# Optimization experiments

Measured on AMD Instinct MI355X. Metric: run time of the kernel, lower is better.

Reference implementation:

```python
import jax, jax.numpy as jnp
import numpy as np

NUM_GROUPS = 32
EPS = 1e-5


def _conv(x, w, b, pad):
    # x: [B,C,H,W], w: [O,I,kh,kw]
    y = jax.lax.conv_general_dilated(
        x, w, window_strides=(1, 1), padding=[(pad, pad), (pad, pad)],
        dimension_numbers=('NCHW', 'OIHW', 'NCHW'))
    return y + b[None, :, None, None]


def _group_norm(x, gamma, beta):
    B, C, H, W = x.shape
    g = x.reshape(B, NUM_GROUPS, C // NUM_GROUPS, H, W)
    mu = g.mean(axis=(2, 3, 4), keepdims=True)
    var = g.var(axis=(2, 3, 4), keepdims=True)
    g = (g - mu) * jax.lax.rsqrt(var + EPS)
    x = g.reshape(B, C, H, W)
    return x * gamma[None, :, None, None] + beta[None, :, None, None]


def setup_inputs() -> dict:
    key = jax.random.key(0)
    ks = jax.random.split(key, 8)
    B, C, H, W = 8, 384, 64, 64
    s1 = 1.0 / np.sqrt(C)          # 1x1 conv fan-in
    s3 = 1.0 / np.sqrt(C * 9)      # 3x3 conv fan-in
    return {
        'x': jax.random.normal(ks[0], (B, C, H, W), dtype=jnp.float32),
        'gamma': jnp.ones((C,), dtype=jnp.float32),
        'beta': jnp.zeros((C,), dtype=jnp.float32),
        'wq': jax.random.normal(ks[1], (C, C, 1, 1), dtype=jnp.float32) * s1,
        'bq': jnp.zeros((C,), dtype=jnp.float32),
        'wk': jax.random.normal(ks[2], (C, C, 3, 3), dtype=jnp.float32) * s3,
        'bk': jnp.zeros((C,), dtype=jnp.float32),
        'wv': jax.random.normal(ks[3], (C, C, 1, 1), dtype=jnp.float32) * s1,
        'bv': jnp.zeros((C,), dtype=jnp.float32),
        'wf': jax.random.normal(ks[4], (C, C, 1, 1), dtype=jnp.float32) * s1,
        'bf': jnp.zeros((C,), dtype=jnp.float32),
        'k': 512,
    }


def reference(x, gamma, beta, wq, bq, wk, bk, wv, bv, wf, bf, k):
    B, C, H, W = x.shape
    xn = _group_norm(x, gamma, beta)
    q = _conv(xn, wq, bq, 0)
    kk = _conv(xn, wk, bk, 1)
    v = _conv(xn, wv, bv, 0)
    # frequency-domain correlation: elementwise product of 2D spectra
    Fq = jnp.fft.fft2(q)
    Fk = jnp.fft.fft2(kk)
    A = jnp.fft.ifft2(Fq * Fk).real          # [B,C,H,W]
    # per-(batch,channel) spatial top-k sparsification
    A_flat = A.reshape(B, C, H * W)
    topv, _ = jax.lax.top_k(A_flat, k)
    thresh = topv[..., -1:]                   # k-th largest value
    masked = jnp.where(A_flat >= thresh, A_flat, -jnp.inf)
    Fw = jax.nn.softmax(masked, axis=-1).reshape(B, C, H, W)
    F4 = v * Fw                               # weighted values
    res = _conv(F4, wf, bf, 0)
    return xn * res
```

## Files before the change

### kernel.cpp

```cpp
#include <hip/hip_runtime.h>
#include <hip/hip_fp16.h>
#include <math.h>

#define CCH  384
#define BATCH 8
#define HWN  4096
#define NG   32
#define CPG  12
#define KSEL 512
#define FFTP 65
#define LP   40

typedef short v8s  __attribute__((ext_vector_type(8)));
typedef float v16f __attribute__((ext_vector_type(16)));

#define MFMA_B16(A_,B_,C_) __builtin_amdgcn_mfma_f32_32x32x16_bf16((A_),(B_),(C_),0,0,0)

__device__ __forceinline__ unsigned br6(unsigned i) {
  return ((i&1u)<<5)|((i&2u)<<3)|((i&4u)<<1)|((i&8u)>>1)|((i&16u)>>3)|((i&32u)>>5);
}
__device__ __forceinline__ unsigned f2key(float f) {
  unsigned u = __float_as_uint(f);
  return (u & 0x80000000u) ? ~u : (u | 0x80000000u);
}
__device__ __forceinline__ float wave_max(float v) {
#pragma unroll
  for (int o = 32; o > 0; o >>= 1) v = fmaxf(v, __shfl_down(v, o, 64));
  return v;
}
__device__ __forceinline__ float wave_sum(float v) {
#pragma unroll
  for (int o = 32; o > 0; o >>= 1) v += __shfl_down(v, o, 64);
  return v;
}
__device__ __forceinline__ unsigned short bf16_rne(float f) {
  unsigned u = __float_as_uint(f);
  return (unsigned short)((u + 0x7fffu + ((u >> 16) & 1u)) >> 16);
}
__device__ __forceinline__ float bf2f(unsigned short h) {
  return __uint_as_float(((unsigned)h) << 16);
}

__global__ __launch_bounds__(256) void stats_kernel(const float* __restrict__ x,
                                                    float2* __restrict__ gs) {
  int b = blockIdx.x >> 5, g = blockIdx.x & 31;
  size_t base = ((size_t)b * CCH + (size_t)g * CPG) * HWN;
  const float4* xp = (const float4*)(x + base);
  int tid = threadIdx.x;
  const int N4 = CPG * HWN / 4;
  float s = 0.f, ss = 0.f;
  for (int i = tid; i < N4; i += 256) {
    float4 v = xp[i];
    s  += (v.x + v.y) + (v.z + v.w);
    ss += (v.x*v.x + v.y*v.y) + (v.z*v.z + v.w*v.w);
  }
  s = wave_sum(s); ss = wave_sum(ss);
  __shared__ float sb[4], qb[4];
  if ((tid & 63) == 0) { sb[tid >> 6] = s; qb[tid >> 6] = ss; }
  __syncthreads();
  if (tid == 0) {
    float S = sb[0]+sb[1]+sb[2]+sb[3], Q = qb[0]+qb[1]+qb[2]+qb[3];
    float inv = 1.0f / (float)(CPG * HWN);
    float mu = S * inv;
    float var = Q * inv - mu * mu;
    gs[blockIdx.x] = make_float2(mu, rsqrtf(var + 1e-5f));
  }
}

__global__ __launch_bounds__(256) void pack_split_k(const float* __restrict__ w,
    unsigned short* __restrict__ hi, unsigned short* __restrict__ lo, int n) {
  int i = blockIdx.x * 256 + threadIdx.x;
  if (i >= n) return;
  float f = w[i];
  unsigned short h = bf16_rne(f);
  hi[i] = h;
  lo[i] = bf16_rne(f - bf2f(h));
}
__global__ __launch_bounds__(256) void pack9_k(const float* __restrict__ w,
    unsigned short* __restrict__ hi, unsigned short* __restrict__ lo) {
  int i = blockIdx.x * 256 + threadIdx.x;
  int r = blockIdx.y;
  float f = w[(size_t)i * 9 + r];
  unsigned short h = bf16_rne(f);
  size_t o = (size_t)r * 147456 + i;
  hi[o] = h;
  lo[o] = bf16_rne(f - bf2f(h));
}

template<int FUSE, int SPLIT>
__global__ __launch_bounds__(256) void trans_kernel(const float* __restrict__ in,
    const float2* __restrict__ gs, const float* __restrict__ gamma,
    const float* __restrict__ beta,
    unsigned short* __restrict__ oh, unsigned short* __restrict__ ol) {
  __shared__ float ts[64][65];
  int tid = threadIdx.x;
  int b = blockIdx.z, c0 = blockIdx.y * 64, p0 = blockIdx.x * 64;
#pragma unroll
  for (int i = 0; i < 4; ++i) {
    int idx = tid + (i << 8);
    int row = idx >> 4, col = (idx & 15) << 2;
    float4 v = *(const float4*)&in[((size_t)b*CCH + c0 + row)*HWN + p0 + col];
    if (FUSE) {
      int c = c0 + row;
      float2 st = gs[(b << 5) + c / CPG];
      float a = gamma[c] * st.y, bb = beta[c] - st.x * a;
      v.x = v.x*a+bb; v.y = v.y*a+bb; v.z = v.z*a+bb; v.w = v.w*a+bb;
    }
    ts[row][col] = v.x; ts[row][col+1] = v.y; ts[row][col+2] = v.z; ts[row][col+3] = v.w;
  }
  __syncthreads();
#pragma unroll
  for (int i = 0; i < 2; ++i) {
    int idx = tid + (i << 8);
    int p = idx >> 3, cgp = (idx & 7) << 3;
    unsigned short h8[8] __attribute__((aligned(16)));
    unsigned short l8[8] __attribute__((aligned(16)));
#pragma unroll
    for (int j = 0; j < 8; ++j) {
      float f = ts[cgp + j][p];
      unsigned short hb = bf16_rne(f);
      h8[j] = hb;
      if (SPLIT) l8[j] = bf16_rne(f - bf2f(hb));
    }
    size_t o = ((size_t)b*HWN + p0 + p)*CCH + c0 + cgp;
    *(uint4*)&oh[o] = *(const uint4*)h8;
    if (SPLIT) *(uint4*)&ol[o] = *(const uint4*)l8;
  }
}

template<int TAPS, int OUT>
__global__ __launch_bounds__(256, 3) void mm_kernel(
    const unsigned short* __restrict__ Ahg, const unsigned short* __restrict__ Alg,
    const float* __restrict__ bias,
    const unsigned short* __restrict__ Bhg, const unsigned short* __restrict__ Blg,
    const unsigned short* __restrict__ xnTh, const unsigned short* __restrict__ xnTl,
    void* __restrict__ Yv) {
  __shared__ unsigned short Ah_s[128*LP], Al_s[128*LP], Bh_s[128*LP], Bl_s[128*LP];
  int tid = threadIdx.x;
  int b = blockIdx.z, m0 = blockIdx.y * 128, n0 = blockIdx.x * 128;
  int y0 = blockIdx.x * 2;
  int u0row = tid >> 2, cg = tid & 3;
  int lds0 = u0row * LP + cg * 8, lds1 = lds0 + 64 * LP;
  size_t aoff0 = (size_t)(m0 + u0row) * CCH + cg * 8;
  int lane = tid & 63, wm = tid >> 7, wn = (tid >> 6) & 1;
  int lm = lane & 31, lh = lane >> 5;
  int arow = (wm * 64 + lm) * LP, brow = (wn * 64 + lm) * LP;

  v16f acc[2][2];
#pragma unroll
  for (int t = 0; t < 2; ++t)
#pragma unroll
    for (int s = 0; s < 2; ++s)
#pragma unroll
      for (int g = 0; g < 16; ++g) acc[t][s][g] = 0.f;

  const int NS = TAPS * 12;
  uint4 ra0h, ra0l, ra1h, ra1l, rb0h, rb0l, rb1h, rb1l;

  auto issue = [&](int s) {
    int r  = (TAPS == 9) ? (s / 12) : 0;
    int c0 = (s - r * 12) * 32;
    const unsigned short* Arh = Ahg + (size_t)r * CCH * CCH + aoff0 + c0;
    const unsigned short* Arl = Alg + (size_t)r * CCH * CCH + aoff0 + c0;
    ra0h = *(const uint4*)Arh;
    ra0l = *(const uint4*)Arl;
    ra1h = *(const uint4*)(Arh + 64 * CCH);
    ra1l = *(const uint4*)(Arl + 64 * CCH);
    int dy = (TAPS == 9) ? r / 3 - 1 : 0;
    int dx = (TAPS == 9) ? r % 3 - 1 : 0;
    int px = u0row + dx;
    int py0 = y0 + dy, py1 = py0 + 1;
    bool okx = (unsigned)px < 64u;
    bool ok0 = okx && ((unsigned)py0 < 64u);
    bool ok1 = okx && ((unsigned)py1 < 64u);
    size_t boff0 = ((size_t)b * HWN + py0 * 64 + px) * CCH + cg * 8 + c0;
    size_t boff1 = ((size_t)b * HWN + py1 * 64 + px) * CCH + cg * 8 + c0;
    uint4 zf; zf.x = zf.y = zf.z = zf.w = 0u;
    rb0h = ok0 ? *(const uint4*)(Bhg + boff0) : zf;
    rb0l = ok0 ? *(const uint4*)(Blg + boff0) : zf;
    rb1h = ok1 ? *(const uint4*)(Bhg + boff1) : zf;
    rb1l = ok1 ? *(const uint4*)(Blg + boff1) : zf;
  };

  issue(0);
  for (int s = 0; s < NS; ++s) {
    __syncthreads();
    *(uint4*)&Ah_s[lds0] = ra0h; *(uint4*)&Al_s[lds0] = ra0l;
    *(uint4*)&Ah_s[lds1] = ra1h; *(uint4*)&Al_s[lds1] = ra1l;
    *(uint4*)&Bh_s[lds0] = rb0h; *(uint4*)&Bl_s[lds0] = rb0l;
    *(uint4*)&Bh_s[lds1] = rb1h; *(uint4*)&Bl_s[lds1] = rb1l;
    __syncthreads();
    if (s + 1 < NS) issue(s + 1);
#pragma unroll
    for (int h = 0; h < 2; ++h) {
      int co = h * 16 + lh * 8;
      v8s a0h = *(const v8s*)&Ah_s[arow + co];
      v8s a1h = *(const v8s*)&Ah_s[arow + 32*LP + co];
      v8s a0l = *(const v8s*)&Al_s[arow + co];
      v8s a1l = *(const v8s*)&Al_s[arow + 32*LP + co];
      v8s b0h = *(const v8s*)&Bh_s[brow + co];
      v8s b1h = *(const v8s*)&Bh_s[brow + 32*LP + co];
      v8s b0l = *(const v8s*)&Bl_s[brow + co];
      v8s b1l = *(const v8s*)&Bl_s[brow + 32*LP + co];
      acc[0][0] = MFMA_B16(a0h, b0h, acc[0][0]);
      acc[0][0] = MFMA_B16(a0h, b0l, acc[0][0]);
      acc[0][0] = MFMA_B16(a0l, b0h, acc[0][0]);
      acc[0][1] = MFMA_B16(a0h, b1h, acc[0][1]);
      acc[0][1] = MFMA_B16(a0h, b1l, acc[0][1]);
      acc[0][1] = MFMA_B16(a0l, b1h, acc[0][1]);
      acc[1][0] = MFMA_B16(a1h, b0h, acc[1][0]);
      acc[1][0] = MFMA_B16(a1h, b0l, acc[1][0]);
      acc[1][0] = MFMA_B16(a1l, b0h, acc[1][0]);
      acc[1][1] = MFMA_B16(a1h, b1h, acc[1][1]);
      acc[1][1] = MFMA_B16(a1h, b1l, acc[1][1]);
      acc[1][1] = MFMA_B16(a1l, b1h, acc[1][1]);
    }
  }
#pragma unroll
  for (int t = 0; t < 2; ++t) {
    int mb = m0 + wm * 64 + t * 32;
#pragma unroll
    for (int s = 0; s < 2; ++s) {
      int n = n0 + wn * 64 + s * 32 + lm;
#pragma unroll
      for (int g = 0; g < 16; ++g) {
        int m = mb + (g & 3) + ((g >> 2) << 3) + (lh << 2);
        float val = acc[t][s][g] + bias[m];
        size_t oidx = ((size_t)b * CCH + m) * HWN + n;
        if (OUT == 0) {
          ((float*)Yv)[oidx] = val;
        } else if (OUT == 1) {
          ((__half*)Yv)[oidx] = __float2half(val);
        } else {
          size_t tix = ((size_t)b * HWN + n) * CCH + m;
          float xnv = bf2f(xnTh[tix]) + bf2f(xnTl[tix]);
          ((float*)Yv)[oidx] = val * xnv;
        }
      }
    }
  }
}

__device__ __forceinline__ void fft4_pass(float* zr, float* zi,
    const float* twr, const float* twi, int tid, int axis, float ds) {
#pragma unroll
  for (int s = 0; s < 3; ++s) {
    const int h = 1 << (2 * s);
#pragma unroll
    for (int tt = 0; tt < 4; ++tt) {
      int t = tid + (tt << 8);
      int line = t >> 4, bf = t & 15;
      int j  = bf & (h - 1);
      int i0 = ((bf >> (2 * s)) << (2 * s + 2)) + j;
      int e1 = j << (5 - 2 * s);
      int e2 = j << (4 - 2 * s);
      float w1r = twr[e1], w1i = ds * twi[e1];
      float w2r = twr[e2], w2i = ds * twi[e2];
      int A0, st;
      if (axis == 0) { A0 = line * FFTP + i0; st = h; }
      else           { A0 = i0 * FFTP + line; st = h * FFTP; }
      int A1 = A0 + st, A2 = A1 + st, A3 = A2 + st;
      float x0r = zr[A0], x0i = zi[A0];
      float x1r = zr[A1], x1i = zi[A1];
      float x2r = zr[A2], x2i = zi[A2];
      float x3r = zr[A3], x3i = zi[A3];
      float t1r = x1r*w1r - x1i*w1i, t1i = x1r*w1i + x1i*w1r;
      float t3r = x3r*w1r - x3i*w1i, t3i = x3r*w1i + x3i*w1r;
      float u0r = x0r + t1r, u0i = x0i + t1i;
      float u1r = x0r - t1r, u1i = x0i - t1i;
      float u2r = x2r + t3r, u2i = x2i + t3i;
      float u3r = x2r - t3r, u3i = x2i - t3i;
      float c2r = u2r*w2r - u2i*w2i, c2i = u2r*w2i + u2i*w2r;
      float c3r = u3r*w2r - u3i*w2i, c3i = u3r*w2i + u3i*w2r;
      zr[A0] = u0r + c2r;      zi[A0] = u0i + c2i;
      zr[A2] = u0r - c2r;      zi[A2] = u0i - c2i;
      zr[A1] = u1r + ds*c3i;   zi[A1] = u1i - ds*c3r;
      zr[A3] = u1r - ds*c3i;   zi[A3] = u1i + ds*c3r;
    }
    __syncthreads();
  }
}

__global__ __launch_bounds__(256) void fft_topk_kernel(
    const float* q, const float* __restrict__ kkb,
    const __half* __restrict__ v, float* F4) {
  __shared__ float zr[64 * FFTP], zi[64 * FFTP];
  __shared__ float twr[32], twi[32];
  __shared__ unsigned hist[256];
  __shared__ unsigned su2[2];
  __shared__ unsigned wtot[4];
  __shared__ float sred[5];
  int tid = threadIdx.x;
  int lane = tid & 63, w = tid >> 6;
  size_t base = (size_t)blockIdx.x * HWN;
  for (int i = tid; i < HWN; i += 256) {
    int y = i >> 6, x = i & 63;
    int slot = br6(y) * FFTP + br6(x);
    zr[slot] = q[base + i];
    zi[slot] = kkb[base + i];
  }
  if (tid < 32) {
    float ang = (float)tid * 0.0981747704246810387f;
    twr[tid] = cosf(ang);
    twi[tid] = -sinf(ang);
  }
  __syncthreads();
  fft4_pass(zr, zi, twr, twi, tid, 0, 1.f);
  fft4_pass(zr, zi, twr, twi, tid, 1, 1.f);
  float prr[16], pir[16];
#pragma unroll
  for (int c = 0; c < 16; c++) {
    int i = tid + (c << 8);
    int ky = i >> 6, kx = i & 63;
    float sr = zr[ky * FFTP + kx], si = zi[ky * FFTP + kx];
    int kyn = (64 - ky) & 63, kxn = (64 - kx) & 63;
    float nr = zr[kyn * FFTP + kxn], ni = zi[kyn * FFTP + kxn];
    float fqr = 0.5f * (sr + nr), fqi = 0.5f * (si - ni);
    float fkr = 0.5f * (si + ni), fki = 0.5f * (nr - sr);
    prr[c] = fqr * fkr - fqi * fki;
    pir[c] = fqr * fki + fqi * fkr;
  }
  __syncthreads();
#pragma unroll
  for (int c = 0; c < 16; c++) {
    int i = tid + (c << 8);
    int ky = i >> 6, kx = i & 63;
    int slot = br6(ky) * FFTP + br6(kx);
    zr[slot] = prr[c];
    zi[slot] = pir[c];
  }
  __syncthreads();
  fft4_pass(zr, zi, twr, twi, tid, 0, -1.f);
  fft4_pass(zr, zi, twr, twi, tid, 1, -1.f);
  const float scale = 1.0f / 4096.0f;
  float a[16];
  unsigned key[16];
  float mx = -3.0e38f;
#pragma unroll
  for (int c = 0; c < 16; c++) {
    int i = tid + (c << 8);
    a[c] = zr[(i >> 6) * FFTP + (i & 63)] * scale;
    key[c] = f2key(a[c]);
    mx = fmaxf(mx, a[c]);
  }
  mx = wave_max(mx);
  if (lane == 0) sred[w] = mx;
  __syncthreads();
  if (tid == 0) sred[4] = fmaxf(fmaxf(sred[0], sred[1]), fmaxf(sred[2], sred[3]));
  __syncthreads();
  float am = sred[4];
  unsigned prefix = 0; int kr = KSEL;
  for (int pass = 0; pass < 4; pass++) {
    int shift = 24 - (pass << 3);
    hist[tid] = 0;
    __syncthreads();
#pragma unroll
    for (int c = 0; c < 16; c++) {
      unsigned u = key[c];
      if (((u ^ prefix) >> shift) <= 0xFFu)
        atomicAdd(&hist[(u >> shift) & 255u], 1u);
    }
    __syncthreads();
    unsigned xv = hist[tid];
#pragma unroll
    for (int o = 1; o < 64; o <<= 1) {
      unsigned t2 = __shfl_down(xv, o, 64);
      if (lane + o < 64) xv += t2;
    }
    if (lane == 0) wtot[w] = xv;
    __syncthreads();
    for (int ww = w + 1; ww < 4; ++ww) xv += wtot[ww];
    hist[tid] = xv;
    __syncthreads();
    unsigned sv = xv;
    unsigned svn = (tid < 255) ? hist[tid + 1] : 0u;
    if (sv >= (unsigned)kr && svn < (unsigned)kr) { su2[0] = (unsigned)tid; su2[1] = svn; }
    __syncthreads();
    prefix |= su2[0] << shift;
    kr -= (int)su2[1];
  }
  unsigned thr = prefix;
  float lsum = 0.f;
#pragma unroll
  for (int c = 0; c < 16; c++)
    if (key[c] >= thr) lsum += expf(a[c] - am);
  lsum = wave_sum(lsum);
  if (lane == 0) sred[w] = lsum;
  __syncthreads();
  if (tid == 0) sred[4] = 1.0f / (sred[0] + sred[1] + sred[2] + sred[3]);
  __syncthreads();
  float inv = sred[4];
#pragma unroll
  for (int c = 0; c < 16; c++) {
    int i = tid + (c << 8);
    float wgt = (key[c] >= thr) ? expf(a[c] - am) * inv : 0.f;
    F4[base + i] = __half2float(v[base + i]) * wgt;
  }
}

extern "C" void kernel_launch(void* const* d_in, const int* in_sizes, int n_in,
                              void* d_out, int out_size, void* d_ws, size_t ws_size,
                              hipStream_t stream) {
  const float* x     = (const float*)d_in[0];
  const float* gamma = (const float*)d_in[1];
  const float* beta  = (const float*)d_in[2];
  const float* wq    = (const float*)d_in[3];
  const float* bq    = (const float*)d_in[4];
  const float* wk    = (const float*)d_in[5];
  const float* bk    = (const float*)d_in[6];
  const float* wv    = (const float*)d_in[7];
  const float* bv    = (const float*)d_in[8];
  const float* wf    = (const float*)d_in[9];
  const float* bf    = (const float*)d_in[10];

  const size_t NEL = (size_t)BATCH * CCH * HWN;
  const size_t WSZ = (size_t)CCH * CCH;

  unsigned short* xnTh = (unsigned short*)d_ws;
  unsigned short* xnTl = xnTh + NEL;
  float*  qC  = (float*)(xnTl + NEL);
  float*  kD  = qC + NEL;
  __half* vE  = (__half*)(kD + NEL);
  unsigned short* W = (unsigned short*)(vE + NEL);
  unsigned short* Wqh = W;
  unsigned short* Wql = Wqh + WSZ;
  unsigned short* Wvh = Wql + WSZ;
  unsigned short* Wvl = Wvh + WSZ;
  unsigned short* Wfh = Wvl + WSZ;
  unsigned short* Wfl = Wfh + WSZ;
  unsigned short* Wkh = Wfl + WSZ;
  unsigned short* Wkl = Wkh + 9 * WSZ;
  float2* gs = (float2*)(Wkl + 9 * WSZ);
  unsigned short* F4Th = (unsigned short*)kD;
  unsigned short* F4Tl = F4Th + NEL;

  pack_split_k<<<dim3(576), dim3(256), 0, stream>>>(wq, Wqh, Wql, (int)WSZ);
  pack_split_k<<<dim3(576), dim3(256), 0, stream>>>(wv, Wvh, Wvl, (int)WSZ);
  pack_split_k<<<dim3(576), dim3(256), 0, stream>>>(wf, Wfh, Wfl, (int)WSZ);
  pack9_k<<<dim3(576, 9), dim3(256), 0, stream>>>(wk, Wkh, Wkl);
  stats_kernel<<<dim3(BATCH * NG), dim3(256), 0, stream>>>(x, gs);
  trans_kernel<1, 1><<<dim3(64, 6, BATCH), dim3(256), 0, stream>>>(
      x, gs, gamma, beta, xnTh, xnTl);

  dim3 gm(32, 3, BATCH);
  mm_kernel<1, 0><<<gm, dim3(256), 0, stream>>>(Wqh, Wql, bq, xnTh, xnTl,
                                                nullptr, nullptr, qC);
  mm_kernel<9, 0><<<gm, dim3(256), 0, stream>>>(Wkh, Wkl, bk, xnTh, xnTl,
                                                nullptr, nullptr, kD);
  mm_kernel<1, 1><<<gm, dim3(256), 0, stream>>>(Wvh, Wvl, bv, xnTh, xnTl,
                                                nullptr, nullptr, vE);

  fft_topk_kernel<<<dim3(BATCH * CCH), dim3(256), 0, stream>>>(qC, kD, vE, qC);

  trans_kernel<0, 1><<<dim3(64, 6, BATCH), dim3(256), 0, stream>>>(
      qC, nullptr, nullptr, nullptr, F4Th, F4Tl);

  mm_kernel<1, 2><<<gm, dim3(256), 0, stream>>>(Wfh, Wfl, bf, F4Th, F4Tl,
                                                xnTh, xnTl, d_out);
}
```

Measured before the change: 694.3 us.

## Pre-pack weights in MFMA fragment order and load A operands straight to registers

Weights are now packed into per-lane MFMA fragment order, so each wave loads its A operands directly from global memory into registers. This removes the A tiles from shared memory and from the per-step LDS store and read traffic. The next step's A fragments are double-buffered in registers through a two-step unrolled loop. This raises register pressure, so the occupancy hint drops from 3 to 2 blocks. A fragments are also loaded separately by each wave rather than shared across waves through LDS.

```diff
diff --git a/kernel.cpp b/kernel.cpp
--- a/kernel.cpp
+++ b/kernel.cpp
@@ -67,24 +67,20 @@
   }
 }
 
-__global__ __launch_bounds__(256) void pack_split_k(const float* __restrict__ w,
-    unsigned short* __restrict__ hi, unsigned short* __restrict__ lo, int n) {
-  int i = blockIdx.x * 256 + threadIdx.x;
-  if (i >= n) return;
-  float f = w[i];
-  unsigned short h = bf16_rne(f);
-  hi[i] = h;
-  lo[i] = bf16_rne(f - bf2f(h));
-}
-__global__ __launch_bounds__(256) void pack9_k(const float* __restrict__ w,
-    unsigned short* __restrict__ hi, unsigned short* __restrict__ lo) {
-  int i = blockIdx.x * 256 + threadIdx.x;
+__global__ __launch_bounds__(256) void pack_frag_k(const float* __restrict__ w,
+    unsigned short* __restrict__ hi, unsigned short* __restrict__ lo, int taps) {
+  int idx = blockIdx.x * 256 + threadIdx.x;
   int r = blockIdx.y;
-  float f = w[(size_t)i * 9 + r];
-  unsigned short h = bf16_rne(f);
-  size_t o = (size_t)r * 147456 + i;
+  int f = idx >> 9;
+  int l = (idx >> 3) & 63, j = idx & 7;
+  int mb = f / 24, kc = f - mb * 24;
+  int m = mb * 32 + (l & 31);
+  int k = kc * 16 + ((l >> 5) << 3) + j;
+  float fv = (taps == 9) ? w[(size_t)(m * CCH + k) * 9 + r] : w[m * CCH + k];
+  unsigned short h = bf16_rne(fv);
+  size_t o = (size_t)r * 147456 + idx;
   hi[o] = h;
-  lo[o] = bf16_rne(f - bf2f(h));
+  lo[o] = bf16_rne(fv - bf2f(h));
 }
 
 template<int FUSE, int SPLIT>
@@ -129,22 +125,22 @@
 }
 
 template<int TAPS, int OUT>
-__global__ __launch_bounds__(256, 3) void mm_kernel(
+__global__ __launch_bounds__(256, 2) void mm_kernel(
     const unsigned short* __restrict__ Ahg, const unsigned short* __restrict__ Alg,
     const float* __restrict__ bias,
     const unsigned short* __restrict__ Bhg, const unsigned short* __restrict__ Blg,
     const unsigned short* __restrict__ xnTh, const unsigned short* __restrict__ xnTl,
     void* __restrict__ Yv) {
-  __shared__ unsigned short Ah_s[128*LP], Al_s[128*LP], Bh_s[128*LP], Bl_s[128*LP];
+  __shared__ unsigned short Bh_s[128*LP], Bl_s[128*LP];
   int tid = threadIdx.x;
   int b = blockIdx.z, m0 = blockIdx.y * 128, n0 = blockIdx.x * 128;
+  int mb0 = blockIdx.y * 4;
   int y0 = blockIdx.x * 2;
   int u0row = tid >> 2, cg = tid & 3;
   int lds0 = u0row * LP + cg * 8, lds1 = lds0 + 64 * LP;
-  size_t aoff0 = (size_t)(m0 + u0row) * CCH + cg * 8;
   int lane = tid & 63, wm = tid >> 7, wn = (tid >> 6) & 1;
   int lm = lane & 31, lh = lane >> 5;
-  int arow = (wm * 64 + lm) * LP, brow = (wn * 64 + lm) * LP;
+  int brow = (wn * 64 + lm) * LP;
 
   v16f acc[2][2];
 #pragma unroll
@@ -155,17 +151,12 @@
       for (int g = 0; g < 16; ++g) acc[t][s][g] = 0.f;
 
   const int NS = TAPS * 12;
-  uint4 ra0h, ra0l, ra1h, ra1l, rb0h, rb0l, rb1h, rb1l;
-
-  auto issue = [&](int s) {
+  uint4 rb0h, rb0l, rb1h, rb1l;
+  v8s A0[8], A1[8];
+
+  auto issueB = [&](int s) {
     int r  = (TAPS == 9) ? (s / 12) : 0;
     int c0 = (s - r * 12) * 32;
-    const unsigned short* Arh = Ahg + (size_t)r * CCH * CCH + aoff0 + c0;
-    const unsigned short* Arl = Alg + (size_t)r * CCH * CCH + aoff0 + c0;
-    ra0h = *(const uint4*)Arh;
-    ra0l = *(const uint4*)Arl;
-    ra1h = *(const uint4*)(Arh + 64 * CCH);
-    ra1l = *(const uint4*)(Arl + 64 * CCH);
     int dy = (TAPS == 9) ? r / 3 - 1 : 0;
     int dx = (TAPS == 9) ? r % 3 - 1 : 0;
     int px = u0row + dx;
@@ -181,41 +172,57 @@
     rb1h = ok1 ? *(const uint4*)(Bhg + boff1) : zf;
     rb1l = ok1 ? *(const uint4*)(Blg + boff1) : zf;
   };
-
-  issue(0);
-  for (int s = 0; s < NS; ++s) {
-    __syncthreads();
-    *(uint4*)&Ah_s[lds0] = ra0h; *(uint4*)&Al_s[lds0] = ra0l;
-    *(uint4*)&Ah_s[lds1] = ra1h; *(uint4*)&Al_s[lds1] = ra1l;
-    *(uint4*)&Bh_s[lds0] = rb0h; *(uint4*)&Bl_s[lds0] = rb0l;
-    *(uint4*)&Bh_s[lds1] = rb1h; *(uint4*)&Bl_s[lds1] = rb1l;
-    __syncthreads();
-    if (s + 1 < NS) issue(s + 1);
-#pragma unroll
-    for (int h = 0; h < 2; ++h) {
-      int co = h * 16 + lh * 8;
-      v8s a0h = *(const v8s*)&Ah_s[arow + co];
-      v8s a1h = *(const v8s*)&Ah_s[arow + 32*LP + co];
-      v8s a0l = *(const v8s*)&Al_s[arow + co];
-      v8s a1l = *(const v8s*)&Al_s[arow + 32*LP + co];
-      v8s b0h = *(const v8s*)&Bh_s[brow + co];
-      v8s b1h = *(const v8s*)&Bh_s[brow + 32*LP + co];
-      v8s b0l = *(const v8s*)&Bl_s[brow + co];
-      v8s b1l = *(const v8s*)&Bl_s[brow + 32*LP + co];
-      acc[0][0] = MFMA_B16(a0h, b0h, acc[0][0]);
-      acc[0][0] = MFMA_B16(a0h, b0l, acc[0][0]);
-      acc[0][0] = MFMA_B16(a0l, b0h, acc[0][0]);
-      acc[0][1] = MFMA_B16(a0h, b1h, acc[0][1]);
-      acc[0][1] = MFMA_B16(a0h, b1l, acc[0][1]);
-      acc[0][1] = MFMA_B16(a0l, b1h, acc[0][1]);
-      acc[1][0] = MFMA_B16(a1h, b0h, acc[1][0]);
-      acc[1][0] = MFMA_B16(a1h, b0l, acc[1][0]);
-      acc[1][0] = MFMA_B16(a1l, b0h, acc[1][0]);
-      acc[1][1] = MFMA_B16(a1h, b1h, acc[1][1]);
-      acc[1][1] = MFMA_B16(a1h, b1l, acc[1][1]);
-      acc[1][1] = MFMA_B16(a1l, b1h, acc[1][1]);
-    }
-  }
+  auto issueA = [&](int s, v8s* An) {
+    int r   = (TAPS == 9) ? (s / 12) : 0;
+    int kc0 = (s - r * 12) * 2;
+#pragma unroll
+    for (int t = 0; t < 2; ++t)
+#pragma unroll
+      for (int h = 0; h < 2; ++h) {
+        size_t f = (size_t)((r * 12 + mb0 + wm * 2 + t) * 24 + kc0 + h);
+        An[(t*2+h)*2+0] = *(const v8s*)(Ahg + (f << 9) + (lane << 3));
+        An[(t*2+h)*2+1] = *(const v8s*)(Alg + (f << 9) + (lane << 3));
+      }
+  };
+
+#define MMSTEP(SS, Acur, Anext)                                              \
+  {                                                                          \
+    __syncthreads();                                                         \
+    *(uint4*)&Bh_s[lds0] = rb0h; *(uint4*)&Bl_s[lds0] = rb0l;                \
+    *(uint4*)&Bh_s[lds1] = rb1h; *(uint4*)&Bl_s[lds1] = rb1l;                \
+    __syncthreads();                                                         \
+    if ((SS) + 1 < NS) { issueB((SS) + 1); issueA((SS) + 1, Anext); }        \
+    _Pragma("unroll")                                                        \
+    for (int h = 0; h < 2; ++h) {                                            \
+      int co = h * 16 + lh * 8;                                              \
+      v8s a0h = Acur[(0*2+h)*2+0], a0l = Acur[(0*2+h)*2+1];                  \
+      v8s a1h = Acur[(1*2+h)*2+0], a1l = Acur[(1*2+h)*2+1];                  \
+      v8s b0h = *(const v8s*)&Bh_s[brow + co];                               \
+      v8s b1h = *(const v8s*)&Bh_s[brow + 32*LP + co];                       \
+      v8s b0l = *(const v8s*)&Bl_s[brow + co];                               \
+      v8s b1l = *(const v8s*)&Bl_s[brow + 32*LP + co];                       \
+      acc[0][0] = MFMA_B16(a0h, b0h, acc[0][0]);                             \
+      acc[0][0] = MFMA_B16(a0h, b0l, acc[0][0]);                             \
+      acc[0][0] = MFMA_B16(a0l, b0h, acc[0][0]);                             \
+      acc[0][1] = MFMA_B16(a0h, b1h, acc[0][1]);                             \
+      acc[0][1] = MFMA_B16(a0h, b1l, acc[0][1]);                             \
+      acc[0][1] = MFMA_B16(a0l, b1h, acc[0][1]);                             \
+      acc[1][0] = MFMA_B16(a1h, b0h, acc[1][0]);                             \
+      acc[1][0] = MFMA_B16(a1h, b0l, acc[1][0]);                             \
+      acc[1][0] = MFMA_B16(a1l, b0h, acc[1][0]);                             \
+      acc[1][1] = MFMA_B16(a1h, b1h, acc[1][1]);                             \
+      acc[1][1] = MFMA_B16(a1h, b1l, acc[1][1]);                             \
+      acc[1][1] = MFMA_B16(a1l, b1h, acc[1][1]);                             \
+    }                                                                        \
+  }
+
+  issueB(0); issueA(0, A0);
+  for (int s = 0; s < NS; s += 2) {
+    MMSTEP(s, A0, A1);
+    MMSTEP(s + 1, A1, A0);
+  }
+#undef MMSTEP
+
 #pragma unroll
   for (int t = 0; t < 2; ++t) {
     int mb = m0 + wm * 64 + t * 32;
@@ -256,14 +263,14 @@
       int e2 = j << (4 - 2 * s);
       float w1r = twr[e1], w1i = ds * twi[e1];
       float w2r = twr[e2], w2i = ds * twi[e2];
-      int A0, st;
-      if (axis == 0) { A0 = line * FFTP + i0; st = h; }
-      else           { A0 = i0 * FFTP + line; st = h * FFTP; }
-      int A1 = A0 + st, A2 = A1 + st, A3 = A2 + st;
-      float x0r = zr[A0], x0i = zi[A0];
-      float x1r = zr[A1], x1i = zi[A1];
-      float x2r = zr[A2], x2i = zi[A2];
-      float x3r = zr[A3], x3i = zi[A3];
+      int A0_, st;
+      if (axis == 0) { A0_ = line * FFTP + i0; st = h; }
+      else           { A0_ = i0 * FFTP + line; st = h * FFTP; }
+      int A1_ = A0_ + st, A2_ = A1_ + st, A3_ = A2_ + st;
+      float x0r = zr[A0_], x0i = zi[A0_];
+      float x1r = zr[A1_], x1i = zi[A1_];
+      float x2r = zr[A2_], x2i = zi[A2_];
+      float x3r = zr[A3_], x3i = zi[A3_];
       float t1r = x1r*w1r - x1i*w1i, t1i = x1r*w1i + x1i*w1r;
       float t3r = x3r*w1r - x3i*w1i, t3i = x3r*w1i + x3i*w1r;
       float u0r = x0r + t1r, u0i = x0i + t1i;
@@ -272,10 +279,10 @@
       float u3r = x2r - t3r, u3i = x2i - t3i;
       float c2r = u2r*w2r - u2i*w2i, c2i = u2r*w2i + u2i*w2r;
       float c3r = u3r*w2r - u3i*w2i, c3i = u3r*w2i + u3i*w2r;
-      zr[A0] = u0r + c2r;      zi[A0] = u0i + c2i;
-      zr[A2] = u0r - c2r;      zi[A2] = u0i - c2i;
-      zr[A1] = u1r + ds*c3i;   zi[A1] = u1i - ds*c3r;
-      zr[A3] = u1r - ds*c3i;   zi[A3] = u1i + ds*c3r;
+      zr[A0_] = u0r + c2r;      zi[A0_] = u0i + c2i;
+      zr[A2_] = u0r - c2r;      zi[A2_] = u0i - c2i;
+      zr[A1_] = u1r + ds*c3i;   zi[A1_] = u1i - ds*c3r;
+      zr[A3_] = u1r - ds*c3i;   zi[A3_] = u1i + ds*c3r;
     }
     __syncthreads();
   }
@@ -434,10 +441,10 @@
   unsigned short* F4Th = (unsigned short*)kD;
   unsigned short* F4Tl = F4Th + NEL;
 
-  pack_split_k<<<dim3(576), dim3(256), 0, stream>>>(wq, Wqh, Wql, (int)WSZ);
-  pack_split_k<<<dim3(576), dim3(256), 0, stream>>>(wv, Wvh, Wvl, (int)WSZ);
-  pack_split_k<<<dim3(576), dim3(256), 0, stream>>>(wf, Wfh, Wfl, (int)WSZ);
-  pack9_k<<<dim3(576, 9), dim3(256), 0, stream>>>(wk, Wkh, Wkl);
+  pack_frag_k<<<dim3(576, 1), dim3(256), 0, stream>>>(wq, Wqh, Wql, 1);
+  pack_frag_k<<<dim3(576, 1), dim3(256), 0, stream>>>(wv, Wvh, Wvl, 1);
+  pack_frag_k<<<dim3(576, 1), dim3(256), 0, stream>>>(wf, Wfh, Wfl, 1);
+  pack_frag_k<<<dim3(576, 9), dim3(256), 0, stream>>>(wk, Wkh, Wkl, 9);
   stats_kernel<<<dim3(BATCH * NG), dim3(256), 0, stream>>>(x, gs);
   trans_kernel<1, 1><<<dim3(64, 6, BATCH), dim3(256), 0, stream>>>(
       x, gs, gamma, beta, xnTh, xnTl);
```

Result: no change. 699.1 us (+0.7%).
